# Kernel tuning notes

Measured on AMD Instinct MI355X. Metric: run time of the kernel, lower is better.

Reference implementation:

```python
import jax, jax.numpy as jnp
import numpy as np

B, T, IN_DIM, D, H, F, L = 16, 64, 128, 512, 8, 2048, 4  # T == DATA_ROUNDS_PER_GAME
HD = D // H
SCALE = 1.0 / np.sqrt(HD)
NEG = -1e9


def setup_inputs() -> dict:
    key = jax.random.key(0)
    ks = jax.random.split(key, 10)
    s = lambda k, shape, fan: (jax.random.normal(k, shape, jnp.float32) * (fan ** -0.5)).astype(jnp.float32)
    return {
        "x": jax.random.normal(ks[0], (B, T, IN_DIM), jnp.float32),
        "fc_w": s(ks[1], (IN_DIM, D), IN_DIM), "fc_b": jnp.zeros((D,), jnp.float32),
        "w_qkv": s(ks[2], (L, D, 3 * D), D), "b_qkv": jnp.zeros((L, 3 * D), jnp.float32),
        "w_o": s(ks[3], (L, D, D), D), "b_o": jnp.zeros((L, D), jnp.float32),
        "ln1_g": jnp.ones((L, D), jnp.float32), "ln1_b": jnp.zeros((L, D), jnp.float32),
        "w_ff1": s(ks[4], (L, D, F), D), "b_ff1": jnp.zeros((L, F), jnp.float32),
        "w_ff2": s(ks[5], (L, F, D), F), "b_ff2": jnp.zeros((L, D), jnp.float32),
        "ln2_g": jnp.ones((L, D), jnp.float32), "ln2_b": jnp.zeros((L, D), jnp.float32),
        "cls_w1": s(ks[6], (D, D // 2), D), "cls_b1": jnp.zeros((D // 2,), jnp.float32),
        "cls_w2": s(ks[7], (D // 2, 2), D // 2), "cls_b2": jnp.zeros((2,), jnp.float32),
    }


def _ln(x, g, b, eps=1e-5):
    m = x.mean(-1, keepdims=True)
    v = ((x - m) ** 2).mean(-1, keepdims=True)
    return (x - m) * jax.lax.rsqrt(v + eps) * g + b


def _encoder(h, bias, w_qkv, b_qkv, w_o, b_o, ln1_g, ln1_b, w_ff1, b_ff1, w_ff2, b_ff2, ln2_g, ln2_b):
    # post-norm TransformerEncoderLayer (PyTorch default), dropout=0
    for l in range(L):
        Bh, Th = h.shape[0], h.shape[1]
        qkv = h @ w_qkv[l] + b_qkv[l]                      # [B,T,3D]
        q, k, v = jnp.split(qkv, 3, axis=-1)
        q = q.reshape(Bh, Th, H, HD)
        k = k.reshape(Bh, Th, H, HD)
        v = v.reshape(Bh, Th, H, HD)
        scores = jnp.einsum('bqhd,bkhd->bhqk', q, k) * SCALE + bias
        attn = jax.nn.softmax(scores, axis=-1)
        o = jnp.einsum('bhqk,bkhd->bqhd', attn, v).reshape(Bh, Th, D)
        h = _ln(h + o @ w_o[l] + b_o[l], ln1_g[l], ln1_b[l])
        ff = jax.nn.relu(h @ w_ff1[l] + b_ff1[l]) @ w_ff2[l] + b_ff2[l]
        h = _ln(h + ff, ln2_g[l], ln2_b[l])
    return h


def reference(x, fc_w, fc_b, w_qkv, b_qkv, w_o, b_o, ln1_g, ln1_b, w_ff1, b_ff1,
              w_ff2, b_ff2, ln2_g, ln2_b, cls_w1, cls_b1, cls_w2, cls_b2):
    h0 = jax.nn.relu(x @ fc_w + fc_b)                       # [B,T,D]

    def per_prefix(i):
        # keys restricted to positions <= i reproduces re-running the encoder
        # on the prefix x[:, :i+1]; we read position i (the prefix's last token).
        keep = jnp.arange(T) <= i
        bias = jnp.where(keep, 0.0, NEG).astype(h0.dtype)[None, None, None, :]  # [1,1,1,T]
        out = _encoder(h0, bias, w_qkv, b_qkv, w_o, b_o, ln1_g, ln1_b,
                       w_ff1, b_ff1, w_ff2, b_ff2, ln2_g, ln2_b)
        return jnp.take(out, i, axis=1)                     # [B,D]

    y = jax.vmap(per_prefix)(jnp.arange(T))                 # [T,B,D]
    y = jnp.transpose(y, (1, 0, 2))                         # [B,T,D]
    z = jax.nn.relu(y @ cls_w1 + cls_b1) @ cls_w2 + cls_b2  # [B,T,2]
    return jax.nn.log_softmax(z, axis=-1)
```

## Files before the change

### kernel.cpp

```cpp
#include <hip/hip_runtime.h>
#include <math.h>

using u16 = unsigned short;
using u32 = unsigned int;

constexpr int Bc = 16;
constexpr int Tc = 64;
constexpr int INc = 128;
constexpr int Dc = 512;
constexpr int Hc = 8;
constexpr int Fc = 2048;
constexpr int Lc = 4;
constexpr float SCALEc = 0.125f;

constexpr int NGc = 3;
constexpr int g_p0[NGc]   = {0, 35, 51};
constexpr int g_np[NGc]   = {35, 16, 13};
constexpr int g_start[NGc]= {0, 12160, 24192};
constexpr int g_M[NGc]    = {12288, 12032, 12672};
constexpr int g_M3[NGc]   = {640, 256, 256};
constexpr int GMAXc = 12672;
constexpr int M3MAXc = 640;
constexpr int VTSc  = GMAXc + 64;

typedef __attribute__((ext_vector_type(8))) short bf16x8;
typedef __attribute__((ext_vector_type(4))) float f32x4;

__device__ __forceinline__ int rowbase(int p) {
  const int q = p >> 3, r = p & 7;
  return 128 * (4 * q * (q + 1) + r * (q + 1));
}

__device__ __forceinline__ float bf2f(u16 u) {
  union { u32 i; float f; } c; c.i = (u32)u << 16; return c.f;
}
__device__ __forceinline__ u16 f2bf(float f) {
  union { float f; u32 u; } c{f};
  u32 r = (c.u + 0x7fffu + ((c.u >> 16) & 1u)) >> 16;
  return (u16)r;
}

template<bool RELU>
__global__ __launch_bounds__(256) void gemm_kernel(
    const float* __restrict__ A, const float* __restrict__ W,
    const float* __restrict__ bias, float* __restrict__ C,
    u16* __restrict__ Cb, int M, int K, int N)
{
  __shared__ float As[128][17];
  __shared__ float Ws[16][64];
  const int tid = threadIdx.x;
  const int tx = tid & 15, ty = tid >> 4;
  const int row0 = blockIdx.y * 128, col0 = blockIdx.x * 64;
  float acc[8][4];
#pragma unroll
  for (int i = 0; i < 8; ++i)
#pragma unroll
    for (int j = 0; j < 4; ++j) acc[i][j] = 0.f;
  const int ar = tid >> 1, ak = (tid & 1) * 8;
  const int wr = tid >> 4, wc = (tid & 15) * 4;
  for (int k0 = 0; k0 < K; k0 += 16) {
    const float* ap = A + (size_t)(row0 + ar) * K + k0 + ak;
    float4 a0 = *(const float4*)ap;
    float4 a1 = *(const float4*)(ap + 4);
    As[ar][ak+0]=a0.x; As[ar][ak+1]=a0.y; As[ar][ak+2]=a0.z; As[ar][ak+3]=a0.w;
    As[ar][ak+4]=a1.x; As[ar][ak+5]=a1.y; As[ar][ak+6]=a1.z; As[ar][ak+7]=a1.w;
    *(float4*)&Ws[wr][wc] = *(const float4*)(W + (size_t)(k0 + wr) * N + col0 + wc);
    __syncthreads();
#pragma unroll
    for (int kk = 0; kk < 16; ++kk) {
      const float4 w4 = *(const float4*)&Ws[kk][tx * 4];
#pragma unroll
      for (int i = 0; i < 8; ++i) {
        const float av = As[ty + 16 * i][kk];
        acc[i][0] += av * w4.x; acc[i][1] += av * w4.y;
        acc[i][2] += av * w4.z; acc[i][3] += av * w4.w;
      }
    }
    __syncthreads();
  }
#pragma unroll
  for (int i = 0; i < 8; ++i) {
    const int r = row0 + ty + 16 * i, c = col0 + tx * 4;
    float4 v;
    v.x = acc[i][0] + bias[c+0]; v.y = acc[i][1] + bias[c+1];
    v.z = acc[i][2] + bias[c+2]; v.w = acc[i][3] + bias[c+3];
    if (RELU) { v.x=fmaxf(v.x,0.f); v.y=fmaxf(v.y,0.f); v.z=fmaxf(v.z,0.f); v.w=fmaxf(v.w,0.f); }
    *(float4*)&C[(size_t)r * N + c] = v;
    uint2 pk;
    pk.x = (u32)f2bf(v.x) | ((u32)f2bf(v.y) << 16);
    pk.y = (u32)f2bf(v.z) | ((u32)f2bf(v.w) << 16);
    *(uint2*)&Cb[(size_t)r * N + c] = pk;
  }
}

__global__ __launch_bounds__(256) void transpose_conv(
    const float* __restrict__ src, u16* __restrict__ dst, int K, int N)
{
  __shared__ float t[32][33];
  const int bx = blockIdx.x * 32;
  const int by = blockIdx.y * 32;
  const int x = threadIdx.x, y = threadIdx.y;
#pragma unroll
  for (int i = 0; i < 32; i += 8) t[y + i][x] = src[(size_t)(by + y + i) * N + bx + x];
  __syncthreads();
#pragma unroll
  for (int i = 0; i < 32; i += 8)
    dst[(size_t)(bx + y + i) * K + by + x] = f2bf(t[x][y + i]);
}

__global__ __launch_bounds__(256) void transpose_v(
    const u16* __restrict__ qkvsrc, u16* __restrict__ vt, int vstride)
{
  __shared__ u16 t[64][65];
  const int r0 = blockIdx.x * 64;
  const int d0 = blockIdx.y * 64;
  const int tid = threadIdx.x;
  const int rr = tid >> 2, cc = (tid & 3) * 16;
  const u16* src = qkvsrc + (size_t)(r0 + rr) * 1536 + 1024 + d0 + cc;
  union { uint4 v; u16 s[8]; } ua, ub;
  ua.v = *(const uint4*)src;
  ub.v = *(const uint4*)(src + 8);
#pragma unroll
  for (int i = 0; i < 8; ++i) { t[rr][cc + i] = ua.s[i]; t[rr][cc + 8 + i] = ub.s[i]; }
  __syncthreads();
  const int dd = tid >> 2, kk = (tid & 3) * 16;
  union { uint4 v; u16 s[8]; } w0, w1;
#pragma unroll
  for (int i = 0; i < 8; ++i) { w0.s[i] = t[kk + i][dd]; w1.s[i] = t[kk + 8 + i][dd]; }
  u16* dst = vt + (size_t)(d0 + dd) * vstride + r0 + kk;
  *(uint4*)dst = w0.v;
  *(uint4*)(dst + 8) = w1.v;
}

__device__ __forceinline__ void stage_tile(const u16* __restrict__ src, int ldk, u16* lds)
{
  const int tid = threadIdx.x;
#pragma unroll
  for (int q = 0; q < 4; ++q) {
    const int p16 = tid + (q << 8);
    const int row = p16 >> 3;
    const int s   = p16 & 7;
    const int k16 = s ^ (row & 7);
    const u16* g = src + (size_t)row * ldk + (k16 << 3);
    __builtin_amdgcn_global_load_lds(
        (const __attribute__((address_space(1))) void*)g,
        (__attribute__((address_space(3))) void*)(lds + (p16 << 3)),
        16, 0, 0);
  }
}

template<bool RELU, bool OUT_BF16>
__global__ __launch_bounds__(256) void gemm_mfma(
    const u16* __restrict__ A, const u16* __restrict__ Wt,
    const float* __restrict__ bias, void* __restrict__ Cout,
    int M, int K, int N)
{
  __shared__ u16 As[2][128 * 64];
  __shared__ u16 Bs[2][128 * 64];

  const int tid  = threadIdx.x;
  const int lane = tid & 63;
  const int wave = tid >> 6;
  const int wr = wave >> 1;
  const int wc = wave & 1;

  const int gx = gridDim.x;
  const int nwg = gx * gridDim.y;
  const int lin = blockIdx.y * gx + blockIdx.x;
  const int qq = nwg >> 3, r8 = nwg & 7;
  const int xcd = lin & 7, pos = lin >> 3;
  const int orig = (xcd < r8) ? (xcd * (qq + 1) + pos)
                              : (r8 * (qq + 1) + (xcd - r8) * qq + pos);
  const int row0 = (orig / gx) * 128;
  const int col0 = (orig % gx) * 128;

  f32x4 acc[4][4];
#pragma unroll
  for (int i = 0; i < 4; ++i)
#pragma unroll
    for (int j = 0; j < 4; ++j) acc[i][j] = f32x4{0.f, 0.f, 0.f, 0.f};

  const int nk = K >> 6;
  const int arow = wr * 64 + (lane & 15);
  const int brow = wc * 64 + (lane & 15);
  const int kq   = lane >> 4;

  stage_tile(A  + (size_t)row0 * K, K, &As[0][0]);
  stage_tile(Wt + (size_t)col0 * K, K, &Bs[0][0]);

  for (int t = 0; t < nk; ++t) {
    const int cur = t & 1;
    if (t + 1 < nk) {
      const int k0 = (t + 1) << 6;
      stage_tile(A  + (size_t)row0 * K + k0, K, &As[cur ^ 1][0]);
      stage_tile(Wt + (size_t)col0 * K + k0, K, &Bs[cur ^ 1][0]);
      asm volatile("s_waitcnt vmcnt(8)\n\ts_barrier" ::: "memory");
    } else {
      asm volatile("s_waitcnt vmcnt(0)\n\ts_barrier" ::: "memory");
    }
    const u16* Ab = &As[cur][0];
    const u16* Bb = &Bs[cur][0];
#pragma unroll
    for (int kk = 0; kk < 2; ++kk) {
      bf16x8 af[4], bfr[4];
      const int c = kk * 4 + kq;
#pragma unroll
      for (int i = 0; i < 4; ++i) {
        const int ra = arow + i * 16;
        af[i]  = *reinterpret_cast<const bf16x8*>(Ab + ra * 64 + ((c ^ (ra & 7)) << 3));
        const int rb = brow + i * 16;
        bfr[i] = *reinterpret_cast<const bf16x8*>(Bb + rb * 64 + ((c ^ (rb & 7)) << 3));
      }
#pragma unroll
      for (int mi = 0; mi < 4; ++mi)
#pragma unroll
        for (int ni = 0; ni < 4; ++ni)
          acc[mi][ni] = __builtin_amdgcn_mfma_f32_16x16x32_bf16(af[mi], bfr[ni], acc[mi][ni], 0, 0, 0);
    }
    asm volatile("s_barrier" ::: "memory");
  }

  const int r0 = row0 + wr * 64 + ((lane >> 4) << 2);
  const int c0 = col0 + wc * 64 + (lane & 15);
#pragma unroll
  for (int mi = 0; mi < 4; ++mi)
#pragma unroll
    for (int ni = 0; ni < 4; ++ni) {
      const int col = c0 + ni * 16;
      const float bsv = bias[col];
#pragma unroll
      for (int j = 0; j < 4; ++j) {
        const int row = r0 + mi * 16 + j;
        float o = acc[mi][ni][j] + bsv;
        if (RELU) o = fmaxf(o, 0.f);
        if (OUT_BF16) ((u16*)Cout)[(size_t)row * N + col] = f2bf(o);
        else          ((float*)Cout)[(size_t)row * N + col] = o;
      }
    }
}

__global__ __launch_bounds__(128) void bcast_kernel(
    const float* __restrict__ h0, float* __restrict__ h, int p0, int gstart)
{
  const int t = blockIdx.x, b = blockIdx.y, p = p0 + blockIdx.z;
  if (t > p) return;
  const int NT8 = (p + 8) & ~7;
  const size_t row = (size_t)(rowbase(p) + b * NT8 + t - gstart);
  ((float4*)(h + row * Dc))[threadIdx.x] =
      ((const float4*)(h0 + ((size_t)(b * 64 + t)) * Dc))[threadIdx.x];
}

template<bool SHARED>
__global__ __launch_bounds__(64) void attn_mfma_kernel(
    const u16* __restrict__ qkv, const u16* __restrict__ vt, int vstride,
    u16* __restrict__ attno, int p0, int gstart)
{
  const int hh = blockIdx.x, b = blockIdx.y, p = p0 + blockIdx.z;
  const int NT = p + 1;
  const int NT8 = (NT + 7) & ~7;
  const int rb = rowbase(p) + b * NT8 - gstart;
  const int sb = SHARED ? (b * 64) : rb;
  const int tid = threadIdx.x;
  const int lc = tid & 15, lg = tid >> 4;

  __shared__ u16 Plds[64][72];
  __shared__ u16 VTl[4096];
  __shared__ float invl[64];

  {
    const u16* vbase = vt + (size_t)(hh * 64) * vstride + sb;
#pragma unroll
    for (int it = 0; it < 8; ++it) {
      const int gi = tid + (it << 6);
      const int dd = gi >> 3, s = gi & 7;
      const u16* src = vbase + (size_t)dd * vstride + ((s ^ (dd & 7)) << 3);
      __builtin_amdgcn_global_load_lds(
          (const __attribute__((address_space(1))) void*)src,
          (__attribute__((address_space(3))) void*)(&VTl[gi << 3]), 16, 0, 0);
    }
  }

  f32x4 st[4][4];
#pragma unroll
  for (int i = 0; i < 4; ++i)
#pragma unroll
    for (int j = 0; j < 4; ++j) st[i][j] = f32x4{0.f, 0.f, 0.f, 0.f};

#pragma unroll
  for (int kt = 0; kt < 2; ++kt) {
    bf16x8 kf[4], qf[4];
#pragma unroll
    for (int t = 0; t < 4; ++t) {
      if (t * 16 < NT) {
        const size_t rbase = (size_t)(sb + t * 16 + lc) * 1536 + hh * 64 + kt * 32 + lg * 8;
        qf[t] = *reinterpret_cast<const bf16x8*>(qkv + rbase);
        kf[t] = *reinterpret_cast<const bf16x8*>(qkv + rbase + 512);
      }
    }
#pragma unroll
    for (int mi = 0; mi < 4; ++mi)
      if (mi * 16 < NT)
#pragma unroll
        for (int ni = 0; ni < 4; ++ni)
          if (ni * 16 < NT)
            st[mi][ni] = __builtin_amdgcn_mfma_f32_16x16x32_bf16(kf[mi], qf[ni], st[mi][ni], 0, 0, 0);
  }

#pragma unroll
  for (int ni = 0; ni < 4; ++ni) {
    float mm = -3.0e38f;
#pragma unroll
    for (int mi = 0; mi < 4; ++mi)
#pragma unroll
      for (int e = 0; e < 4; ++e)
        if (16 * mi + 4 * lg + e < NT) mm = fmaxf(mm, st[mi][ni][e]);
    mm = fmaxf(mm, __shfl_xor(mm, 16));
    mm = fmaxf(mm, __shfl_xor(mm, 32));
    float ss = 0.f;
#pragma unroll
    for (int mi = 0; mi < 4; ++mi) {
      u16 pb[4];
#pragma unroll
      for (int e = 0; e < 4; ++e) {
        const float pe = (16 * mi + 4 * lg + e < NT)
                           ? __expf((st[mi][ni][e] - mm) * SCALEc) : 0.f;
        ss += pe;
        pb[e] = f2bf(pe);
      }
      uint2 pk;
      pk.x = (u32)pb[0] | ((u32)pb[1] << 16);
      pk.y = (u32)pb[2] | ((u32)pb[3] << 16);
      *reinterpret_cast<uint2*>(&Plds[16 * ni + lc][16 * mi + 4 * lg]) = pk;
    }
    ss += __shfl_xor(ss, 16);
    ss += __shfl_xor(ss, 32);
    if (lg == 0) invl[16 * ni + lc] = 1.f / ss;
  }

  asm volatile("s_waitcnt vmcnt(0)" ::: "memory");
  __syncthreads();

  f32x4 oc[4][4];
#pragma unroll
  for (int i = 0; i < 4; ++i)
#pragma unroll
    for (int j = 0; j < 4; ++j) oc[i][j] = f32x4{0.f, 0.f, 0.f, 0.f};

#pragma unroll
  for (int kt = 0; kt < 2; ++kt) {
    if (kt * 32 < NT) {
      bf16x8 pa[4], vbf[4];
#pragma unroll
      for (int t = 0; t < 4; ++t) {
        if (t * 16 < NT)
          pa[t] = *reinterpret_cast<const bf16x8*>(&Plds[t * 16 + lc][kt * 32 + lg * 8]);
        const int dd = t * 16 + lc;
        vbf[t] = *reinterpret_cast<const bf16x8*>(
            &VTl[dd * 64 + (((4 * kt + lg) ^ (lc & 7)) << 3)]);
      }
#pragma unroll
      for (int qt = 0; qt < 4; ++qt)
        if (qt * 16 < NT)
#pragma unroll
          for (int dt = 0; dt < 4; ++dt)
            oc[qt][dt] = __builtin_amdgcn_mfma_f32_16x16x32_bf16(pa[qt], vbf[dt], oc[qt][dt], 0, 0, 0);
    }
  }

#pragma unroll
  for (int qt = 0; qt < 4; ++qt) {
    if (qt * 16 < NT) {
#pragma unroll
      for (int e = 0; e < 4; ++e) {
        const int qrow = qt * 16 + 4 * lg + e;
        if (qrow < NT) {
          const float inv = invl[qrow];
          u16* dst = attno + (size_t)(rb + qrow) * Dc + hh * 64 + lc;
#pragma unroll
          for (int dt = 0; dt < 4; ++dt)
            dst[dt * 16] = f2bf(oc[qt][dt][e] * inv);
        }
      }
    }
  }
}

__global__ __launch_bounds__(64) void attn_diag_kernel(
    const u16* __restrict__ kv3, const u16* __restrict__ qd,
    u16* __restrict__ attno_d, int p0, int gstart)
{
  const int hh = blockIdx.x, b = blockIdx.y, pl = blockIdx.z;
  const int p = p0 + pl;
  const int NT = p + 1;
  const int NT8 = (NT + 7) & ~7;
  const int rb = rowbase(p) + b * NT8 - gstart;
  const int tid = threadIdx.x;
  const int rd = pl * 16 + b;

  __shared__ u16 Ks[64][64];
  __shared__ u16 Vs[64][64];

  const int lrow = tid >> 3;
  const int lc8  = tid & 7;
  for (int t0 = 0; t0 < NT; t0 += 8) {
    const int tr = rb + t0 + lrow;
    const int csrc = (lc8 ^ lrow) << 3;
    const u16* gk = kv3 + (size_t)tr * 1024 + hh * 64 + csrc;
    const u16* gv = kv3 + (size_t)tr * 1024 + 512 + hh * 64 + csrc;
    __builtin_amdgcn_global_load_lds(
        (const __attribute__((address_space(1))) void*)gk,
        (__attribute__((address_space(3))) void*)(&Ks[t0][0] + tid * 8), 16, 0, 0);
    __builtin_amdgcn_global_load_lds(
        (const __attribute__((address_space(1))) void*)gv,
        (__attribute__((address_space(3))) void*)(&Vs[t0][0] + tid * 8), 16, 0, 0);
  }

  const u16* qp = qd + (size_t)rd * Dc + hh * 64;
  float qv[64];
#pragma unroll
  for (int c8 = 0; c8 < 8; ++c8) {
    const bf16x8 q8 = *reinterpret_cast<const bf16x8*>(qp + c8 * 8);
#pragma unroll
    for (int i = 0; i < 8; ++i) qv[c8 * 8 + i] = bf2f((u16)q8[i]);
  }
  asm volatile("s_waitcnt vmcnt(0)" ::: "memory");
  __syncthreads();

  float dot = -1e30f;
  if (tid < NT) {
    dot = 0.f;
#pragma unroll
    for (int c8 = 0; c8 < 8; ++c8) {
      const bf16x8 k8 = *reinterpret_cast<const bf16x8*>(
          &Ks[tid][0] + ((c8 ^ (tid & 7)) << 3));
#pragma unroll
      for (int i = 0; i < 8; ++i) dot += qv[c8 * 8 + i] * bf2f((u16)k8[i]);
    }
    dot *= SCALEc;
  }
  float mm = dot;
#pragma unroll
  for (int off = 32; off; off >>= 1) mm = fmaxf(mm, __shfl_xor(mm, off));
  const float pt = __expf(dot - mm);
  float s = pt;
#pragma unroll
  for (int off = 32; off; off >>= 1) s += __shfl_xor(s, off);
  const float inv = 1.f / s;

  float o = 0.f;
  for (int t = 0; t < NT; ++t) {
    const float ptt = __shfl(pt, t);
    o += ptt * bf2f(Vs[t][(((tid >> 3) ^ (t & 7)) << 3) + (tid & 7)]);
  }
  attno_d[(size_t)rd * Dc + hh * 64 + tid] = f2bf(o * inv);
}

__device__ inline float wave_sum(float v) {
#pragma unroll
  for (int off = 32; off; off >>= 1) v += __shfl_xor(v, off);
  return v;
}

__global__ __launch_bounds__(256) void res_ln_kernel(
    float* __restrict__ h, u16* __restrict__ hb, const u16* __restrict__ tmpb,
    const float* __restrict__ g, const float* __restrict__ bt)
{
  const size_t row = (size_t)blockIdx.x * 4 + (threadIdx.x >> 6);
  const int t = threadIdx.x & 63;
  float v[8];
  float s = 0.f;
#pragma unroll
  for (int i = 0; i < 8; ++i) {
    v[i] = h[row * Dc + i * 64 + t] + bf2f(tmpb[row * Dc + i * 64 + t]);
    s += v[i];
  }
  s = wave_sum(s);
  const float mean = s * (1.f / 512.f);
  float vs = 0.f;
#pragma unroll
  for (int i = 0; i < 8; ++i) { const float d = v[i] - mean; vs += d * d; }
  vs = wave_sum(vs);
  const float rstd = rsqrtf(vs * (1.f / 512.f) + 1e-5f);
#pragma unroll
  for (int i = 0; i < 8; ++i) {
    const float o = (v[i] - mean) * rstd * g[i * 64 + t] + bt[i * 64 + t];
    h[row * Dc + i * 64 + t] = o;
    hb[row * Dc + i * 64 + t] = f2bf(o);
  }
}

__global__ __launch_bounds__(128) void gather_diag(
    const float* __restrict__ h, float* __restrict__ hd, u16* __restrict__ hbd,
    int p0, int gstart)
{
  const int pl = blockIdx.x >> 4, b = blockIdx.x & 15;
  const int p = p0 + pl;
  const int NT8 = (p + 8) & ~7;
  const size_t src = (size_t)(rowbase(p) + b * NT8 + p - gstart);
  const float4 v = ((const float4*)(h + src * Dc))[threadIdx.x];
  ((float4*)(hd + (size_t)blockIdx.x * Dc))[threadIdx.x] = v;
  uint2 pk;
  pk.x = (u32)f2bf(v.x) | ((u32)f2bf(v.y) << 16);
  pk.y = (u32)f2bf(v.z) | ((u32)f2bf(v.w) << 16);
  ((uint2*)(hbd + (size_t)blockIdx.x * Dc))[threadIdx.x] = pk;
}

__global__ __launch_bounds__(128) void scatter_out(
    const float* __restrict__ hd, float* __restrict__ yb, int p0)
{
  const int pl = blockIdx.x >> 4, b = blockIdx.x & 15;
  const int p = p0 + pl;
  ((float4*)(yb + ((size_t)(b * 64 + p)) * Dc))[threadIdx.x] =
      ((const float4*)(hd + (size_t)blockIdx.x * Dc))[threadIdx.x];
}

__global__ __launch_bounds__(256) void cls_kernel(
    const float* __restrict__ y, const float* __restrict__ w1, const float* __restrict__ b1,
    const float* __restrict__ w2, const float* __restrict__ b2, float* __restrict__ out)
{
  const int row = blockIdx.x;
  const int j = threadIdx.x;
  __shared__ float ys[512];
  ys[j]       = y[(size_t)row * Dc + j];
  ys[j + 256] = y[(size_t)row * Dc + 256 + j];
  __syncthreads();

  float acc = b1[j];
  for (int d = 0; d < 512; ++d) acc += ys[d] * w1[(size_t)d * 256 + j];
  acc = fmaxf(acc, 0.f);

  float c0 = acc * w2[j * 2 + 0];
  float c1 = acc * w2[j * 2 + 1];
  c0 = wave_sum(c0);
  c1 = wave_sum(c1);

  __shared__ float r0[4], r1[4];
  const int w = j >> 6, lane = j & 63;
  if (lane == 0) { r0[w] = c0; r1[w] = c1; }
  __syncthreads();
  if (j == 0) {
    const float z0 = r0[0] + r0[1] + r0[2] + r0[3] + b2[0];
    const float z1 = r1[0] + r1[1] + r1[2] + r1[3] + b2[1];
    const float mz = fmaxf(z0, z1);
    const float lse = mz + logf(expf(z0 - mz) + expf(z1 - mz));
    out[row * 2 + 0] = z0 - lse;
    out[row * 2 + 1] = z1 - lse;
  }
}

extern "C" void kernel_launch(void* const* d_in, const int* in_sizes, int n_in,
                              void* d_out, int out_size, void* d_ws, size_t ws_size,
                              hipStream_t stream)
{
  if (n_in < 19) return;
  const float* x      = (const float*)d_in[0];
  const float* fc_w   = (const float*)d_in[1];
  const float* fc_b   = (const float*)d_in[2];
  const float* w_qkv  = (const float*)d_in[3];
  const float* b_qkv  = (const float*)d_in[4];
  const float* w_o    = (const float*)d_in[5];
  const float* b_o    = (const float*)d_in[6];
  const float* ln1_g  = (const float*)d_in[7];
  const float* ln1_b  = (const float*)d_in[8];
  const float* w_ff1  = (const float*)d_in[9];
  const float* b_ff1  = (const float*)d_in[10];
  const float* w_ff2  = (const float*)d_in[11];
  const float* b_ff2  = (const float*)d_in[12];
  const float* ln2_g  = (const float*)d_in[13];
  const float* ln2_b  = (const float*)d_in[14];
  const float* cls_w1 = (const float*)d_in[15];
  const float* cls_b1 = (const float*)d_in[16];
  const float* cls_w2 = (const float*)d_in[17];
  const float* cls_b2 = (const float*)d_in[18];
  float* out = (float*)d_out;

  char* wp = (char*)d_ws;
  auto alloc = [&](size_t bytes) -> char* {
    char* p = wp; wp += (bytes + 255) & ~(size_t)255; return p;
  };
  float* h0  = (float*)alloc((size_t)Bc * Tc * Dc * 4);
  u16*   h0b = (u16*)  alloc((size_t)Bc * Tc * Dc * 2);
  float* yb  = (float*)alloc((size_t)Bc * Tc * Dc * 4);
  u16*   qkv0= (u16*)  alloc((size_t)Bc * Tc * 3 * Dc * 2);
  u16*   vt0 = (u16*)  alloc((size_t)Dc * Bc * Tc * 2);
  u16 *wtq[Lc], *wto[Lc], *wtf1[Lc], *wtf2[Lc];
  for (int l = 0; l < Lc; ++l) {
    wtq[l]  = (u16*)alloc((size_t)3 * Dc * Dc * 2);
    wto[l]  = (u16*)alloc((size_t)Dc * Dc * 2);
    wtf1[l] = (u16*)alloc((size_t)Fc * Dc * 2);
    wtf2[l] = (u16*)alloc((size_t)Dc * Fc * 2);
  }
  const size_t RS = (size_t)GMAXc + 64;
  float* h     = (float*)alloc((size_t)GMAXc * Dc * 4);
  u16*   hb    = (u16*)  alloc((size_t)GMAXc * Dc * 2);
  u16*   qkvb  = (u16*)  alloc(RS * 3 * Dc * 2);
  u16*   attno = (u16*)  alloc((size_t)GMAXc * Dc * 2);
  u16*   tmpb  = (u16*)  alloc((size_t)GMAXc * Dc * 2);
  u16*   ffb   = (u16*)  alloc((size_t)GMAXc * Fc * 2);
  u16*   vt    = (u16*)  alloc((size_t)Dc * VTSc * 2);
  float* hdiag = (float*)alloc((size_t)M3MAXc * Dc * 4);
  u16*   hbdiag= (u16*)  alloc((size_t)M3MAXc * Dc * 2);
  u16*   attnd = (u16*)  alloc((size_t)M3MAXc * Dc * 2);
  u16*   qd    = (u16*)  alloc((size_t)M3MAXc * Dc * 2);
  if ((size_t)(wp - (char*)d_ws) > ws_size) return;
  u16* kv3 = qkvb;

  const dim3 tb(32, 8);
  for (int l = 0; l < Lc; ++l) {
    transpose_conv<<<dim3(3 * Dc / 32, Dc / 32), tb, 0, stream>>>(
        w_qkv + (size_t)l * Dc * 3 * Dc, wtq[l], Dc, 3 * Dc);
    transpose_conv<<<dim3(Dc / 32, Dc / 32), tb, 0, stream>>>(
        w_o + (size_t)l * Dc * Dc, wto[l], Dc, Dc);
    transpose_conv<<<dim3(Fc / 32, Dc / 32), tb, 0, stream>>>(
        w_ff1 + (size_t)l * Dc * Fc, wtf1[l], Dc, Fc);
    transpose_conv<<<dim3(Dc / 32, Fc / 32), tb, 0, stream>>>(
        w_ff2 + (size_t)l * Fc * Dc, wtf2[l], Fc, Dc);
  }

  gemm_kernel<true><<<dim3(Dc / 64, (Bc * Tc) / 128), 256, 0, stream>>>(
      x, fc_w, fc_b, h0, h0b, Bc * Tc, INc, Dc);

  gemm_mfma<false, true><<<dim3(3 * Dc / 128, (Bc * Tc) / 128), 256, 0, stream>>>(
      h0b, wtq[0], b_qkv, qkv0, Bc * Tc, Dc, 3 * Dc);
  transpose_v<<<dim3((Bc * Tc) / 64, 8), 256, 0, stream>>>(qkv0, vt0, Bc * Tc);

  for (int g = 0; g < NGc; ++g) {
    const int p0 = g_p0[g], np = g_np[g], gs = g_start[g], Mg = g_M[g];
    const int M3 = g_M3[g];

    bcast_kernel<<<dim3(64, 16, np), 128, 0, stream>>>(h0, h, p0, gs);

    attn_mfma_kernel<true><<<dim3(Hc, Bc, np), 64, 0, stream>>>(
        qkv0, vt0, Bc * Tc, attno, p0, gs);
    gemm_mfma<false, true><<<dim3(Dc / 128, Mg / 128), 256, 0, stream>>>(
        attno, wto[0], b_o, tmpb, Mg, Dc, Dc);
    res_ln_kernel<<<Mg / 4, 256, 0, stream>>>(h, hb, tmpb, ln1_g, ln1_b);
    gemm_mfma<true, true><<<dim3(Fc / 128, Mg / 128), 256, 0, stream>>>(
        hb, wtf1[0], b_ff1, ffb, Mg, Dc, Fc);
    gemm_mfma<false, true><<<dim3(Dc / 128, Mg / 128), 256, 0, stream>>>(
        ffb, wtf2[0], b_ff2, tmpb, Mg, Fc, Dc);
    res_ln_kernel<<<Mg / 4, 256, 0, stream>>>(h, hb, tmpb, ln2_g, ln2_b);

    for (int l = 1; l < 3; ++l) {
      gemm_mfma<false, true><<<dim3(3 * Dc / 128, Mg / 128), 256, 0, stream>>>(
          hb, wtq[l], b_qkv + (size_t)l * 3 * Dc, qkvb, Mg, Dc, 3 * Dc);
      transpose_v<<<dim3(Mg / 64, 8), 256, 0, stream>>>(qkvb, vt, VTSc);
      attn_mfma_kernel<false><<<dim3(Hc, Bc, np), 64, 0, stream>>>(
          qkvb, vt, VTSc, attno, p0, gs);
      gemm_mfma<false, true><<<dim3(Dc / 128, Mg / 128), 256, 0, stream>>>(
          attno, wto[l], b_o + (size_t)l * Dc, tmpb, Mg, Dc, Dc);
      res_ln_kernel<<<Mg / 4, 256, 0, stream>>>(h, hb, tmpb, ln1_g + l * Dc, ln1_b + l * Dc);
      gemm_mfma<true, true><<<dim3(Fc / 128, Mg / 128), 256, 0, stream>>>(
          hb, wtf1[l], b_ff1 + (size_t)l * Fc, ffb, Mg, Dc, Fc);
      gemm_mfma<false, true><<<dim3(Dc / 128, Mg / 128), 256, 0, stream>>>(
          ffb, wtf2[l], b_ff2 + (size_t)l * Dc, tmpb, Mg, Fc, Dc);
      res_ln_kernel<<<Mg / 4, 256, 0, stream>>>(h, hb, tmpb, ln2_g + l * Dc, ln2_b + l * Dc);
    }

    {
      const int l = 3;
      gather_diag<<<np * 16, 128, 0, stream>>>(h, hdiag, hbdiag, p0, gs);
      gemm_mfma<false, true><<<dim3(Dc / 128, M3 / 128), 256, 0, stream>>>(
          hbdiag, wtq[l], b_qkv + (size_t)l * 3 * Dc, qd, M3, Dc, Dc);
      gemm_mfma<false, true><<<dim3(2 * Dc / 128, Mg / 128), 256, 0, stream>>>(
          hb, wtq[l] + (size_t)512 * Dc, b_qkv + (size_t)l * 3 * Dc + 512,
          kv3, Mg, Dc, 2 * Dc);
      attn_diag_kernel<<<dim3(Hc, Bc, np), 64, 0, stream>>>(kv3, qd, attnd, p0, gs);
      gemm_mfma<false, true><<<dim3(Dc / 128, M3 / 128), 256, 0, stream>>>(
          attnd, wto[l], b_o + (size_t)l * Dc, tmpb, M3, Dc, Dc);
      res_ln_kernel<<<M3 / 4, 256, 0, stream>>>(hdiag, hbdiag, tmpb, ln1_g + l * Dc, ln1_b + l * Dc);
      gemm_mfma<true, true><<<dim3(Fc / 128, M3 / 128), 256, 0, stream>>>(
          hbdiag, wtf1[l], b_ff1 + (size_t)l * Fc, ffb, M3, Dc, Fc);
      gemm_mfma<false, true><<<dim3(Dc / 128, M3 / 128), 256, 0, stream>>>(
          ffb, wtf2[l], b_ff2 + (size_t)l * Dc, tmpb, M3, Fc, Dc);
      res_ln_kernel<<<M3 / 4, 256, 0, stream>>>(hdiag, hbdiag, tmpb, ln2_g + l * Dc, ln2_b + l * Dc);
      scatter_out<<<np * 16, 128, 0, stream>>>(hdiag, yb, p0);
    }
  }

  cls_kernel<<<Bc * Tc, 256, 0, stream>>>(yb, cls_w1, cls_b1, cls_w2, cls_b2, out);
}
```

Before: 1.822 ms.

## Switch GEMM to triple-buffered 32-wide K tiles with two-stage prefetch

New measurement: 1.996 ms. 9.5% more time.

```diff
diff --git a/kernel.cpp b/kernel.cpp
--- a/kernel.cpp
+++ b/kernel.cpp
@@ -132,15 +132,15 @@
   *(uint4*)(dst + 8) = w1.v;
 }
 
-__device__ __forceinline__ void stage_tile(const u16* __restrict__ src, int ldk, u16* lds)
+__device__ __forceinline__ void stage_tile32(const u16* __restrict__ src, int ldk, u16* lds)
 {
   const int tid = threadIdx.x;
 #pragma unroll
-  for (int q = 0; q < 4; ++q) {
+  for (int q = 0; q < 2; ++q) {
     const int p16 = tid + (q << 8);
-    const int row = p16 >> 3;
-    const int s   = p16 & 7;
-    const int k16 = s ^ (row & 7);
+    const int row = p16 >> 2;
+    const int s   = p16 & 3;
+    const int k16 = s ^ (row & 3);
     const u16* g = src + (size_t)row * ldk + (k16 << 3);
     __builtin_amdgcn_global_load_lds(
         (const __attribute__((address_space(1))) void*)g,
@@ -155,8 +155,8 @@
     const float* __restrict__ bias, void* __restrict__ Cout,
     int M, int K, int N)
 {
-  __shared__ u16 As[2][128 * 64];
-  __shared__ u16 Bs[2][128 * 64];
+  __shared__ u16 As[3 * 128 * 32];
+  __shared__ u16 Bs[3 * 128 * 32];
 
   const int tid  = threadIdx.x;
   const int lane = tid & 63;
@@ -180,44 +180,49 @@
 #pragma unroll
     for (int j = 0; j < 4; ++j) acc[i][j] = f32x4{0.f, 0.f, 0.f, 0.f};
 
-  const int nk = K >> 6;
+  const int nk = K >> 5;
   const int arow = wr * 64 + (lane & 15);
   const int brow = wc * 64 + (lane & 15);
   const int kq   = lane >> 4;
 
-  stage_tile(A  + (size_t)row0 * K, K, &As[0][0]);
-  stage_tile(Wt + (size_t)col0 * K, K, &Bs[0][0]);
-
+  const u16* Abase = A  + (size_t)row0 * K;
+  const u16* Bbase = Wt + (size_t)col0 * K;
+
+  stage_tile32(Abase, K, &As[0]);
+  stage_tile32(Bbase, K, &Bs[0]);
+  stage_tile32(Abase + 32, K, &As[128 * 32]);
+  stage_tile32(Bbase + 32, K, &Bs[128 * 32]);
+
+  int cur = 0, nb = 2;
   for (int t = 0; t < nk; ++t) {
-    const int cur = t & 1;
-    if (t + 1 < nk) {
-      const int k0 = (t + 1) << 6;
-      stage_tile(A  + (size_t)row0 * K + k0, K, &As[cur ^ 1][0]);
-      stage_tile(Wt + (size_t)col0 * K + k0, K, &Bs[cur ^ 1][0]);
+    if (t + 2 < nk) {
+      const int k0 = (t + 2) << 5;
+      stage_tile32(Abase + k0, K, &As[nb * (128 * 32)]);
+      stage_tile32(Bbase + k0, K, &Bs[nb * (128 * 32)]);
       asm volatile("s_waitcnt vmcnt(8)\n\ts_barrier" ::: "memory");
+    } else if (t + 1 < nk) {
+      asm volatile("s_waitcnt vmcnt(4)\n\ts_barrier" ::: "memory");
     } else {
       asm volatile("s_waitcnt vmcnt(0)\n\ts_barrier" ::: "memory");
     }
-    const u16* Ab = &As[cur][0];
-    const u16* Bb = &Bs[cur][0];
-#pragma unroll
-    for (int kk = 0; kk < 2; ++kk) {
-      bf16x8 af[4], bfr[4];
-      const int c = kk * 4 + kq;
-#pragma unroll
-      for (int i = 0; i < 4; ++i) {
-        const int ra = arow + i * 16;
-        af[i]  = *reinterpret_cast<const bf16x8*>(Ab + ra * 64 + ((c ^ (ra & 7)) << 3));
-        const int rb = brow + i * 16;
-        bfr[i] = *reinterpret_cast<const bf16x8*>(Bb + rb * 64 + ((c ^ (rb & 7)) << 3));
-      }
-#pragma unroll
-      for (int mi = 0; mi < 4; ++mi)
-#pragma unroll
-        for (int ni = 0; ni < 4; ++ni)
-          acc[mi][ni] = __builtin_amdgcn_mfma_f32_16x16x32_bf16(af[mi], bfr[ni], acc[mi][ni], 0, 0, 0);
-    }
+    const u16* Ab = &As[cur * (128 * 32)];
+    const u16* Bb = &Bs[cur * (128 * 32)];
+    bf16x8 af[4], bfr[4];
+#pragma unroll
+    for (int i = 0; i < 4; ++i) {
+      const int ra = arow + i * 16;
+      af[i]  = *reinterpret_cast<const bf16x8*>(Ab + ra * 32 + ((kq ^ (ra & 3)) << 3));
+      const int rb = brow + i * 16;
+      bfr[i] = *reinterpret_cast<const bf16x8*>(Bb + rb * 32 + ((kq ^ (rb & 3)) << 3));
+    }
+#pragma unroll
+    for (int mi = 0; mi < 4; ++mi)
+#pragma unroll
+      for (int ni = 0; ni < 4; ++ni)
+        acc[mi][ni] = __builtin_amdgcn_mfma_f32_16x16x32_bf16(af[mi], bfr[ni], acc[mi][ni], 0, 0, 0);
     asm volatile("s_barrier" ::: "memory");
+    cur = (cur == 2) ? 0 : cur + 1;
+    nb  = (nb == 2) ? 0 : nb + 1;
   }
 
   const int r0 = row0 + wr * 64 + ((lane >> 4) << 2);
```

## Batch last-layer diagonal tail across groups and fuse broadcast into first LayerNorm

Applied to the files above, without the earlier changes.

After: 1.687 ms. -7.4%, faster.

```diff
diff --git a/kernel.cpp b/kernel.cpp
--- a/kernel.cpp
+++ b/kernel.cpp
@@ -19,8 +19,10 @@
 constexpr int g_start[NGc]= {0, 12160, 24192};
 constexpr int g_M[NGc]    = {12288, 12032, 12672};
 constexpr int g_M3[NGc]   = {640, 256, 256};
+constexpr int g_doff[NGc] = {0, 560, 816};
 constexpr int GMAXc = 12672;
-constexpr int M3MAXc = 640;
+constexpr int DALLc = 1024;
+constexpr int DPADc = 1152;
 constexpr int VTSc  = GMAXc + 64;
 
 typedef __attribute__((ext_vector_type(8))) short bf16x8;
@@ -239,17 +241,6 @@
     }
 }
 
-__global__ __launch_bounds__(128) void bcast_kernel(
-    const float* __restrict__ h0, float* __restrict__ h, int p0, int gstart)
-{
-  const int t = blockIdx.x, b = blockIdx.y, p = p0 + blockIdx.z;
-  if (t > p) return;
-  const int NT8 = (p + 8) & ~7;
-  const size_t row = (size_t)(rowbase(p) + b * NT8 + t - gstart);
-  ((float4*)(h + row * Dc))[threadIdx.x] =
-      ((const float4*)(h0 + ((size_t)(b * 64 + t)) * Dc))[threadIdx.x];
-}
-
 template<bool SHARED>
 __global__ __launch_bounds__(64) void attn_mfma_kernel(
     const u16* __restrict__ qkv, const u16* __restrict__ vt, int vstride,
@@ -387,7 +378,7 @@
 
 __global__ __launch_bounds__(64) void attn_diag_kernel(
     const u16* __restrict__ kv3, const u16* __restrict__ qd,
-    u16* __restrict__ attno_d, int p0, int gstart)
+    u16* __restrict__ attno_d, int p0, int gstart, int doff)
 {
   const int hh = blockIdx.x, b = blockIdx.y, pl = blockIdx.z;
   const int p = p0 + pl;
@@ -395,7 +386,7 @@
   const int NT8 = (NT + 7) & ~7;
   const int rb = rowbase(p) + b * NT8 - gstart;
   const int tid = threadIdx.x;
-  const int rd = pl * 16 + b;
+  const int rd = doff + pl * 16 + b;
 
   __shared__ u16 Ks[64][64];
   __shared__ u16 Vs[64][64];
@@ -489,29 +480,63 @@
   }
 }
 
+__global__ __launch_bounds__(64) void res_ln0_kernel(
+    const float* __restrict__ h0, float* __restrict__ h, u16* __restrict__ hb,
+    const u16* __restrict__ tmpb, const float* __restrict__ g,
+    const float* __restrict__ bt, int p0, int gstart)
+{
+  const int t = blockIdx.x, b = blockIdx.y, p = p0 + blockIdx.z;
+  if (t > p) return;
+  const int NT8 = (p + 8) & ~7;
+  const size_t row = (size_t)(rowbase(p) + b * NT8 + t - gstart);
+  const int tt = threadIdx.x;
+  const float* src = h0 + (size_t)(b * 64 + t) * Dc;
+  float v[8];
+  float s = 0.f;
+#pragma unroll
+  for (int i = 0; i < 8; ++i) {
+    v[i] = src[i * 64 + tt] + bf2f(tmpb[row * Dc + i * 64 + tt]);
+    s += v[i];
+  }
+  s = wave_sum(s);
+  const float mean = s * (1.f / 512.f);
+  float vs = 0.f;
+#pragma unroll
+  for (int i = 0; i < 8; ++i) { const float d = v[i] - mean; vs += d * d; }
+  vs = wave_sum(vs);
+  const float rstd = rsqrtf(vs * (1.f / 512.f) + 1e-5f);
+#pragma unroll
+  for (int i = 0; i < 8; ++i) {
+    const float o = (v[i] - mean) * rstd * g[i * 64 + tt] + bt[i * 64 + tt];
+    h[row * Dc + i * 64 + tt] = o;
+    hb[row * Dc + i * 64 + tt] = f2bf(o);
+  }
+}
+
 __global__ __launch_bounds__(128) void gather_diag(
     const float* __restrict__ h, float* __restrict__ hd, u16* __restrict__ hbd,
-    int p0, int gstart)
+    int p0, int gstart, int doff)
 {
   const int pl = blockIdx.x >> 4, b = blockIdx.x & 15;
   const int p = p0 + pl;
   const int NT8 = (p + 8) & ~7;
   const size_t src = (size_t)(rowbase(p) + b * NT8 + p - gstart);
+  const size_t rd = doff + blockIdx.x;
   const float4 v = ((const float4*)(h + src * Dc))[threadIdx.x];
-  ((float4*)(hd + (size_t)blockIdx.x * Dc))[threadIdx.x] = v;
+  ((float4*)(hd + rd * Dc))[threadIdx.x] = v;
   uint2 pk;
   pk.x = (u32)f2bf(v.x) | ((u32)f2bf(v.y) << 16);
   pk.y = (u32)f2bf(v.z) | ((u32)f2bf(v.w) << 16);
-  ((uint2*)(hbd + (size_t)blockIdx.x * Dc))[threadIdx.x] = pk;
+  ((uint2*)(hbd + rd * Dc))[threadIdx.x] = pk;
 }
 
 __global__ __launch_bounds__(128) void scatter_out(
-    const float* __restrict__ hd, float* __restrict__ yb, int p0)
+    const float* __restrict__ hd, float* __restrict__ yb, int p0, int doff)
 {
   const int pl = blockIdx.x >> 4, b = blockIdx.x & 15;
   const int p = p0 + pl;
   ((float4*)(yb + ((size_t)(b * 64 + p)) * Dc))[threadIdx.x] =
-      ((const float4*)(hd + (size_t)blockIdx.x * Dc))[threadIdx.x];
+      ((const float4*)(hd + (size_t)(doff + blockIdx.x) * Dc))[threadIdx.x];
 }
 
 __global__ __launch_bounds__(256) void cls_kernel(
@@ -598,10 +623,10 @@
   u16*   tmpb  = (u16*)  alloc((size_t)GMAXc * Dc * 2);
   u16*   ffb   = (u16*)  alloc((size_t)GMAXc * Fc * 2);
   u16*   vt    = (u16*)  alloc((size_t)Dc * VTSc * 2);
-  float* hdiag = (float*)alloc((size_t)M3MAXc * Dc * 4);
-  u16*   hbdiag= (u16*)  alloc((size_t)M3MAXc * Dc * 2);
-  u16*   attnd = (u16*)  alloc((size_t)M3MAXc * Dc * 2);
-  u16*   qd    = (u16*)  alloc((size_t)M3MAXc * Dc * 2);
+  float* hdiag = (float*)alloc((size_t)DPADc * Dc * 4);
+  u16*   hbdiag= (u16*)  alloc((size_t)DPADc * Dc * 2);
+  u16*   attnd = (u16*)  alloc((size_t)DPADc * Dc * 2);
+  u16*   qd    = (u16*)  alloc((size_t)DPADc * Dc * 2);
   if ((size_t)(wp - (char*)d_ws) > ws_size) return;
   u16* kv3 = qkvb;
 
@@ -626,15 +651,14 @@
 
   for (int g = 0; g < NGc; ++g) {
     const int p0 = g_p0[g], np = g_np[g], gs = g_start[g], Mg = g_M[g];
-    const int M3 = g_M3[g];
-
-    bcast_kernel<<<dim3(64, 16, np), 128, 0, stream>>>(h0, h, p0, gs);
+    const int M3 = g_M3[g], doff = g_doff[g];
 
     attn_mfma_kernel<true><<<dim3(Hc, Bc, np), 64, 0, stream>>>(
         qkv0, vt0, Bc * Tc, attno, p0, gs);
     gemm_mfma<false, true><<<dim3(Dc / 128, Mg / 128), 256, 0, stream>>>(
         attno, wto[0], b_o, tmpb, Mg, Dc, Dc);
-    res_ln_kernel<<<Mg / 4, 256, 0, stream>>>(h, hb, tmpb, ln1_g, ln1_b);
+    res_ln0_kernel<<<dim3(64, 16, np), 64, 0, stream>>>(
+        h0, h, hb, tmpb, ln1_g, ln1_b, p0, gs);
     gemm_mfma<true, true><<<dim3(Fc / 128, Mg / 128), 256, 0, stream>>>(
         hb, wtf1[0], b_ff1, ffb, Mg, Dc, Fc);
     gemm_mfma<false, true><<<dim3(Dc / 128, Mg / 128), 256, 0, stream>>>(
@@ -659,23 +683,32 @@
 
     {
       const int l = 3;
-      gather_diag<<<np * 16, 128, 0, stream>>>(h, hdiag, hbdiag, p0, gs);
+      gather_diag<<<np * 16, 128, 0, stream>>>(h, hdiag, hbdiag, p0, gs, doff);
       gemm_mfma<false, true><<<dim3(Dc / 128, M3 / 128), 256, 0, stream>>>(
-          hbdiag, wtq[l], b_qkv + (size_t)l * 3 * Dc, qd, M3, Dc, Dc);
+          hbdiag + (size_t)doff * Dc, wtq[l], b_qkv + (size_t)l * 3 * Dc,
+          qd + (size_t)doff * Dc, M3, Dc, Dc);
       gemm_mfma<false, true><<<dim3(2 * Dc / 128, Mg / 128), 256, 0, stream>>>(
           hb, wtq[l] + (size_t)512 * Dc, b_qkv + (size_t)l * 3 * Dc + 512,
           kv3, Mg, Dc, 2 * Dc);
-      attn_diag_kernel<<<dim3(Hc, Bc, np), 64, 0, stream>>>(kv3, qd, attnd, p0, gs);
-      gemm_mfma<false, true><<<dim3(Dc / 128, M3 / 128), 256, 0, stream>>>(
-          attnd, wto[l], b_o + (size_t)l * Dc, tmpb, M3, Dc, Dc);
-      res_ln_kernel<<<M3 / 4, 256, 0, stream>>>(hdiag, hbdiag, tmpb, ln1_g + l * Dc, ln1_b + l * Dc);
-      gemm_mfma<true, true><<<dim3(Fc / 128, M3 / 128), 256, 0, stream>>>(
-          hbdiag, wtf1[l], b_ff1 + (size_t)l * Fc, ffb, M3, Dc, Fc);
-      gemm_mfma<false, true><<<dim3(Dc / 128, M3 / 128), 256, 0, stream>>>(
-          ffb, wtf2[l], b_ff2 + (size_t)l * Dc, tmpb, M3, Fc, Dc);
-      res_ln_kernel<<<M3 / 4, 256, 0, stream>>>(hdiag, hbdiag, tmpb, ln2_g + l * Dc, ln2_b + l * Dc);
-      scatter_out<<<np * 16, 128, 0, stream>>>(hdiag, yb, p0);
-    }
+      attn_diag_kernel<<<dim3(Hc, Bc, np), 64, 0, stream>>>(
+          kv3, qd, attnd, p0, gs, doff);
+    }
+  }
+
+  {
+    const int l = 3;
+    gemm_mfma<false, true><<<dim3(Dc / 128, DALLc / 128), 256, 0, stream>>>(
+        attnd, wto[l], b_o + (size_t)l * Dc, tmpb, DALLc, Dc, Dc);
+    res_ln_kernel<<<DALLc / 4, 256, 0, stream>>>(hdiag, hbdiag, tmpb,
+                                                 ln1_g + l * Dc, ln1_b + l * Dc);
+    gemm_mfma<true, true><<<dim3(Fc / 128, DALLc / 128), 256, 0, stream>>>(
+        hbdiag, wtf1[l], b_ff1 + (size_t)l * Fc, ffb, DALLc, Dc, Fc);
+    gemm_mfma<false, true><<<dim3(Dc / 128, DALLc / 128), 256, 0, stream>>>(
+        ffb, wtf2[l], b_ff2 + (size_t)l * Dc, tmpb, DALLc, Fc, Dc);
+    res_ln_kernel<<<DALLc / 4, 256, 0, stream>>>(hdiag, hbdiag, tmpb,
+                                                 ln2_g + l * Dc, ln2_b + l * Dc);
+    for (int g = 0; g < NGc; ++g)
+      scatter_out<<<g_np[g] * 16, 128, 0, stream>>>(hdiag, yb, g_p0[g], g_doff[g]);
   }
 
   cls_kernel<<<Bc * Tc, 256, 0, stream>>>(yb, cls_w1, cls_b1, cls_w2, cls_b2, out);
```
